# Kernel optimization log

Hardware: AMD Instinct MI355X
Metric: run time of the kernel (lower is better)

## Reference

```python
import jax, jax.numpy as jnp
import numpy as np

GAMMA = 0.015625  # 1/D


def setup_inputs() -> dict:
    key = jax.random.key(0)
    k1, k2 = jax.random.split(key)
    data = jax.random.normal(k1, (8192, 64), dtype=jnp.float32)
    support_vectors = jax.random.normal(k2, (8192, 64), dtype=jnp.float32)
    return {"data": data, "support_vectors": support_vectors}


def reference(data, support_vectors):
    # RBF kernel matrix: K[i,j] = exp(-gamma * ||data_i - sv_j||^2)
    # instead of the original per-row Python loop.
    x_sq = jnp.sum(data * data, axis=1, keepdims=True)          # [N, 1]
    y_sq = jnp.sum(support_vectors * support_vectors, axis=1)   # [M]
    cross = data @ support_vectors.T                             # [N, M]
    d2 = jnp.maximum(x_sq + y_sq[None, :] - 2.0 * cross, 0.0)
    return jnp.exp(-GAMMA * d2)
```

## Files before the change

### kernel.cpp

```cpp
#include <hip/hip_runtime.h>
#include <hip/hip_bf16.h>
#include <string.h>

#define GAMMA 0.015625f
#define D 64

typedef short bf16x8 __attribute__((ext_vector_type(8)));
typedef float floatx4 __attribute__((ext_vector_type(4)));

__global__ __launch_bounds__(256) void prep_kernel(const float* __restrict__ src,
                                                   short* __restrict__ dst,
                                                   float* __restrict__ norms,
                                                   int nrows) {
    int wave = threadIdx.x >> 6;
    int lane = threadIdx.x & 63;
    int row  = blockIdx.x * 4 + wave;
    if (row >= nrows) return;
    float v = src[(size_t)row * D + lane];
    __hip_bfloat16 b = __float2bfloat16(v);
    short bs;
    memcpy(&bs, &b, sizeof(short));
    dst[(size_t)row * D + lane] = bs;
    float bv = __bfloat162float(b);
    float sq = bv * bv;
#pragma unroll
    for (int off = 32; off > 0; off >>= 1) sq += __shfl_down(sq, off, 64);
    if (lane == 0) norms[row] = sq;
}

__global__ __launch_bounds__(256) void rbf_gemm(const short* __restrict__ A,
                                                const short* __restrict__ B,
                                                const float* __restrict__ xsq,
                                                const float* __restrict__ ysq,
                                                float* __restrict__ out,
                                                int M) {
    const int wid  = threadIdx.x >> 6;
    const int lane = threadIdx.x & 63;
    const int quad = lane >> 4;
    const int l16  = lane & 15;

    const long row0 = (long)blockIdx.y * 128 + (wid >> 1) * 64;
    const long col0 = (long)blockIdx.x * 128 + (wid & 1) * 64;

    bf16x8 af[4][2], bfr[4][2];
#pragma unroll
    for (int mb = 0; mb < 4; ++mb) {
        const bf16x8* p = (const bf16x8*)(A + (row0 + mb * 16 + l16) * D + quad * 8);
        af[mb][0] = p[0];
        af[mb][1] = p[4];
    }
#pragma unroll
    for (int nb = 0; nb < 4; ++nb) {
        const bf16x8* p = (const bf16x8*)(B + (col0 + nb * 16 + l16) * D + quad * 8);
        bfr[nb][0] = p[0];
        bfr[nb][1] = p[4];
    }

    floatx4 acc[4][4];
#pragma unroll
    for (int mb = 0; mb < 4; ++mb)
#pragma unroll
        for (int nb = 0; nb < 4; ++nb)
            acc[mb][nb] = (floatx4){0.f, 0.f, 0.f, 0.f};

#pragma unroll
    for (int k = 0; k < 2; ++k)
#pragma unroll
        for (int mb = 0; mb < 4; ++mb)
#pragma unroll
            for (int nb = 0; nb < 4; ++nb)
                acc[mb][nb] = __builtin_amdgcn_mfma_f32_16x16x32_bf16(
                    af[mb][k], bfr[nb][k], acc[mb][nb], 0, 0, 0);

#pragma unroll
    for (int mb = 0; mb < 4; ++mb) {
        const float4 xn4 = *(const float4*)(xsq + row0 + mb * 16 + quad * 4);
        const float xn[4] = {xn4.x, xn4.y, xn4.z, xn4.w};
#pragma unroll
        for (int nb = 0; nb < 4; ++nb) {
            const long col = col0 + nb * 16 + l16;
            const float yn = ysq[col];
#pragma unroll
            for (int r = 0; r < 4; ++r) {
                const long row = row0 + mb * 16 + quad * 4 + r;
                float d2 = fmaxf(xn[r] + yn - 2.0f * acc[mb][nb][r], 0.0f);
                out[row * (long)M + col] = __expf(-GAMMA * d2);
            }
        }
    }
}

__global__ __launch_bounds__(256) void rbf_naive(const float* __restrict__ X,
                                                 const float* __restrict__ Y,
                                                 float* __restrict__ out,
                                                 int N, int M) {
    long idx = (long)blockIdx.x * blockDim.x + threadIdx.x;
    if (idx >= (long)N * M) return;
    long i = idx / M, j = idx % M;
    float s = 0.0f;
#pragma unroll
    for (int k = 0; k < D; ++k) {
        float d = X[i * D + k] - Y[j * D + k];
        s = fmaf(d, d, s);
    }
    out[idx] = __expf(-GAMMA * s);
}

extern "C" void kernel_launch(void* const* d_in, const int* in_sizes, int n_in,
                              void* d_out, int out_size, void* d_ws, size_t ws_size,
                              hipStream_t stream) {
    const float* data = (const float*)d_in[0];
    const float* sv   = (const float*)d_in[1];
    float* out = (float*)d_out;
    const int N = in_sizes[0] / D;
    const int M = in_sizes[1] / D;

    const size_t bfA   = (size_t)N * D * sizeof(short);
    const size_t bfB   = (size_t)M * D * sizeof(short);
    const size_t nrmA  = (size_t)N * sizeof(float);
    const size_t nrmB  = (size_t)M * sizeof(float);
    const size_t need  = bfA + bfB + nrmA + nrmB;

    if (ws_size >= need && (N % 128) == 0 && (M % 128) == 0) {
        char* ws = (char*)d_ws;
        short* Abf = (short*)ws;
        short* Bbf = (short*)(ws + bfA);
        float* xsq = (float*)(ws + bfA + bfB);
        float* ysq = xsq + N;

        hipLaunchKernelGGL(prep_kernel, dim3((N + 3) / 4), dim3(256), 0, stream,
                           data, Abf, xsq, N);
        hipLaunchKernelGGL(prep_kernel, dim3((M + 3) / 4), dim3(256), 0, stream,
                           sv, Bbf, ysq, M);
        dim3 grid(M / 128, N / 128);
        hipLaunchKernelGGL(rbf_gemm, grid, dim3(256), 0, stream,
                           Abf, Bbf, xsq, ysq, out, M);
    } else {
        long total = (long)N * M;
        long blocks = (total + 255) / 256;
        hipLaunchKernelGGL(rbf_naive, dim3((unsigned)blocks), dim3(256), 0, stream,
                           data, sv, out, N, M);
    }
}
```

Before: 272.3 us.

## Fuse bf16 conversion and norm computation into the RBF GEMM kernel

Removes the two prep kernels that converted inputs to bf16 and computed row norms in a workspace. The GEMM kernel now loads fp32 rows directly, converts them to bf16 in registers, and computes the squared norms with cross-lane shuffles. This saves two launches and the workspace round trip. In exchange, each tile redundantly rereads and reconverts fp32 input, doubling input read bytes per tile, though the output write of 256MB dominates.

```diff
diff --git a/kernel.cpp b/kernel.cpp
--- a/kernel.cpp
+++ b/kernel.cpp
@@ -8,32 +8,27 @@
 typedef short bf16x8 __attribute__((ext_vector_type(8)));
 typedef float floatx4 __attribute__((ext_vector_type(4)));
 
-__global__ __launch_bounds__(256) void prep_kernel(const float* __restrict__ src,
-                                                   short* __restrict__ dst,
-                                                   float* __restrict__ norms,
-                                                   int nrows) {
-    int wave = threadIdx.x >> 6;
-    int lane = threadIdx.x & 63;
-    int row  = blockIdx.x * 4 + wave;
-    if (row >= nrows) return;
-    float v = src[(size_t)row * D + lane];
-    __hip_bfloat16 b = __float2bfloat16(v);
-    short bs;
-    memcpy(&bs, &b, sizeof(short));
-    dst[(size_t)row * D + lane] = bs;
-    float bv = __bfloat162float(b);
-    float sq = bv * bv;
+__device__ __forceinline__ bf16x8 cvt8(const float* __restrict__ p, float& ss) {
+    const float4 a = *(const float4*)p;
+    const float4 b = *(const float4*)(p + 4);
+    const float f[8] = {a.x, a.y, a.z, a.w, b.x, b.y, b.z, b.w};
+    bf16x8 r;
 #pragma unroll
-    for (int off = 32; off > 0; off >>= 1) sq += __shfl_down(sq, off, 64);
-    if (lane == 0) norms[row] = sq;
+    for (int i = 0; i < 8; ++i) {
+        __hip_bfloat16 h = __float2bfloat16(f[i]);
+        short s;
+        memcpy(&s, &h, sizeof(short));
+        r[i] = s;
+        const float bv = __bfloat162float(h);
+        ss = fmaf(bv, bv, ss);
+    }
+    return r;
 }
 
-__global__ __launch_bounds__(256) void rbf_gemm(const short* __restrict__ A,
-                                                const short* __restrict__ B,
-                                                const float* __restrict__ xsq,
-                                                const float* __restrict__ ysq,
-                                                float* __restrict__ out,
-                                                int M) {
+__global__ __launch_bounds__(256) void rbf_fused(const float* __restrict__ A,
+                                                 const float* __restrict__ B,
+                                                 float* __restrict__ out,
+                                                 int M) {
     const int wid  = threadIdx.x >> 6;
     const int lane = threadIdx.x & 63;
     const int quad = lane >> 4;
@@ -43,17 +38,28 @@
     const long col0 = (long)blockIdx.x * 128 + (wid & 1) * 64;
 
     bf16x8 af[4][2], bfr[4][2];
+    float xnorm[4];
+    float ynorm[4];
+
 #pragma unroll
     for (int mb = 0; mb < 4; ++mb) {
-        const bf16x8* p = (const bf16x8*)(A + (row0 + mb * 16 + l16) * D + quad * 8);
-        af[mb][0] = p[0];
-        af[mb][1] = p[4];
+        const float* p = A + (row0 + mb * 16 + l16) * D + quad * 8;
+        float s = 0.f;
+        af[mb][0] = cvt8(p, s);
+        af[mb][1] = cvt8(p + 32, s);
+        s += __shfl_xor(s, 16, 64);
+        s += __shfl_xor(s, 32, 64);
+        xnorm[mb] = s;
     }
 #pragma unroll
     for (int nb = 0; nb < 4; ++nb) {
-        const bf16x8* p = (const bf16x8*)(B + (col0 + nb * 16 + l16) * D + quad * 8);
-        bfr[nb][0] = p[0];
-        bfr[nb][1] = p[4];
+        const float* p = B + (col0 + nb * 16 + l16) * D + quad * 8;
+        float s = 0.f;
+        bfr[nb][0] = cvt8(p, s);
+        bfr[nb][1] = cvt8(p + 32, s);
+        s += __shfl_xor(s, 16, 64);
+        s += __shfl_xor(s, 32, 64);
+        ynorm[nb] = s;
     }
 
     floatx4 acc[4][4];
@@ -74,12 +80,14 @@
 
 #pragma unroll
     for (int mb = 0; mb < 4; ++mb) {
-        const float4 xn4 = *(const float4*)(xsq + row0 + mb * 16 + quad * 4);
-        const float xn[4] = {xn4.x, xn4.y, xn4.z, xn4.w};
+        float xn[4];
+#pragma unroll
+        for (int r = 0; r < 4; ++r)
+            xn[r] = __shfl(xnorm[mb], quad * 4 + r, 64);
 #pragma unroll
         for (int nb = 0; nb < 4; ++nb) {
             const long col = col0 + nb * 16 + l16;
-            const float yn = ysq[col];
+            const float yn = ynorm[nb];
 #pragma unroll
             for (int r = 0; r < 4; ++r) {
                 const long row = row0 + mb * 16 + quad * 4 + r;
@@ -115,26 +123,10 @@
     const int N = in_sizes[0] / D;
     const int M = in_sizes[1] / D;
 
-    const size_t bfA   = (size_t)N * D * sizeof(short);
-    const size_t bfB   = (size_t)M * D * sizeof(short);
-    const size_t nrmA  = (size_t)N * sizeof(float);
-    const size_t nrmB  = (size_t)M * sizeof(float);
-    const size_t need  = bfA + bfB + nrmA + nrmB;
-
-    if (ws_size >= need && (N % 128) == 0 && (M % 128) == 0) {
-        char* ws = (char*)d_ws;
-        short* Abf = (short*)ws;
-        short* Bbf = (short*)(ws + bfA);
-        float* xsq = (float*)(ws + bfA + bfB);
-        float* ysq = xsq + N;
-
-        hipLaunchKernelGGL(prep_kernel, dim3((N + 3) / 4), dim3(256), 0, stream,
-                           data, Abf, xsq, N);
-        hipLaunchKernelGGL(prep_kernel, dim3((M + 3) / 4), dim3(256), 0, stream,
-                           sv, Bbf, ysq, M);
+    if ((N % 128) == 0 && (M % 128) == 0) {
         dim3 grid(M / 128, N / 128);
-        hipLaunchKernelGGL(rbf_gemm, grid, dim3(256), 0, stream,
-                           Abf, Bbf, xsq, ysq, out, M);
+        hipLaunchKernelGGL(rbf_fused, grid, dim3(256), 0, stream,
+                           data, sv, out, M);
     } else {
         long total = (long)N * M;
         long blocks = (total + 255) / 256;
```

Result: slower. 303.6 us (+11.5%).
